# Performance work log

Measured on AMD Instinct MI355X. Metric: run time of the kernel, lower is better.

## Reference

```python
import jax, jax.numpy as jnp
import numpy as np


def setup_inputs() -> dict:
    key = jax.random.key(0)
    k1, k2, k3 = jax.random.split(key, 3)
    B, S, D = 4, 2048, 1024   # batch, seq_len, hidden
    M = 65536                 # external memory size
    x = jax.random.normal(k1, (B, S, D), dtype=jnp.float32)
    keys = jax.random.normal(k2, (M, D), dtype=jnp.float32)
    vals = jax.random.normal(k3, (M, D), dtype=jnp.float32)
    return {"x": x, "ver": 1, "keys": keys, "vals": vals}


def reference(x, ver, keys, vals):
    # linear_attention: unnormalized attention over external memory.
    #   out = (x @ keys^T) @ vals
    # Use associativity to avoid materializing the [B,S,M] score matrix:
    #   kv = keys^T @ vals  -> [D, D]
    kv = jnp.einsum("md,me->de", keys, vals)   # [D, D]
    out = jnp.einsum("bsd,de->bse", x, kv)      # [B, S, D]
    return out
```

## Files before the change

### kernel.cpp

```cpp
#include <hip/hip_runtime.h>
#include <hip/hip_bf16.h>


typedef __attribute__((ext_vector_type(8))) __bf16 bf16x8;
typedef __attribute__((ext_vector_type(4))) __bf16 bf16x4;
typedef __attribute__((ext_vector_type(4))) float  f32x4;

#define D_DIM   1024
#define M_DIM   65536
#define ROWS    8192
#define NCHUNK  16
#define MC      (M_DIM / NCHUNK)
#define BT      128
#define BK      64
#define LDK     72
#define TILE_BYTES 16384

__device__ __forceinline__ f32x4 mfma16(bf16x8 a, bf16x8 b, f32x4 c) {
    return __builtin_amdgcn_mfma_f32_16x16x32_bf16(a, b, c, 0, 0, 0);
}

__device__ __forceinline__ void gl_lds16(const void* gsrc, void* ldst) {
    __builtin_amdgcn_global_load_lds(
        (const __attribute__((address_space(1))) unsigned int*)gsrc,
        (__attribute__((address_space(3))) unsigned int*)ldst,
        16, 0, 0);
}

__global__ __launch_bounds__(256)
void convert_tile(const float* __restrict__ keys,
                  const float* __restrict__ vals,
                  __hip_bfloat16* __restrict__ KtT,
                  __hip_bfloat16* __restrict__ VtT)
{
    const float* src = blockIdx.z ? vals : keys;
    char* dstb = (char*)(blockIdx.z ? VtT : KtT);

    const int tid = threadIdx.x;
    const int s   = blockIdx.x;
    const int dq  = blockIdx.y;
    const int m0  = s * 64;
    const int d0  = dq * 256;

    const int q   = tid & 15;
    const int dcb = tid >> 4;

    const int cl   = q >> 1;
    const int half = (q & 1) << 3;

    f32x4 v[4][4];
    #pragma unroll
    for (int i = 0; i < 4; ++i) {
        const int dc = dcb + 16 * i;
        #pragma unroll
        for (int r = 0; r < 4; ++r)
            v[i][r] = *(const f32x4*)(src + (size_t)(m0 + 4 * q + r) * D_DIM + d0 + 4 * dc);
    }

    #pragma unroll
    for (int i = 0; i < 4; ++i) {
        const int dc = dcb + 16 * i;
        #pragma unroll
        for (int j = 0; j < 4; ++j) {
            bf16x4 w;
            #pragma unroll
            for (int r = 0; r < 4; ++r) w[r] = (__bf16)v[i][r][j];
            const int d  = 4 * dc + j;
            const int t  = dq * 2 + (d >> 7);
            const int dl = d & 127;
            char* tile = dstb + ((size_t)t * 1024 + s) * TILE_BYTES;
            *(bf16x4*)(tile + dl * 128 + ((cl ^ (dl & 7)) << 4) + half) = w;
        }
    }
}

__global__ __launch_bounds__(256)
void convert_rows(const float* __restrict__ src,
                  __hip_bfloat16* __restrict__ dstT)
{
    const int tid = threadIdx.x;
    const int rt  = blockIdx.x;
    const int t   = blockIdx.y;
    const int r0  = rt * 128, d0 = t * 64;
    char* tile = (char*)dstT + ((size_t)rt * 16 + t) * TILE_BYTES;
    #pragma unroll
    for (int it = 0; it < 4; ++it) {
        const int idx = tid + it * 256;
        const int r   = idx >> 3;
        const int cl  = idx & 7;
        const float* p = src + (size_t)(r0 + r) * D_DIM + d0 + cl * 8;
        f32x4 a = *(const f32x4*)p;
        f32x4 b = *(const f32x4*)(p + 4);
        bf16x8 w;
        w[0] = (__bf16)a[0]; w[1] = (__bf16)a[1]; w[2] = (__bf16)a[2]; w[3] = (__bf16)a[3];
        w[4] = (__bf16)b[0]; w[5] = (__bf16)b[1]; w[6] = (__bf16)b[2]; w[7] = (__bf16)b[3];
        *(bf16x8*)(tile + r * 128 + ((cl ^ (r & 7)) * 16)) = w;
    }
}

__global__ __launch_bounds__(512, 2)
void kv_gemm8(const __hip_bfloat16* __restrict__ VtT,
              const __hip_bfloat16* __restrict__ KtT,
              float* __restrict__ kvw)
{
    __shared__ __align__(16) char lds[2][4][TILE_BYTES];

    const int tid  = threadIdx.x;
    const int lane = tid & 63;
    const int wave = tid >> 6;
    const int we   = wave >> 2;
    const int wd   = wave & 3;

    const int bx    = blockIdx.x;
    const int xcd   = bx & 7;
    const int idx   = bx >> 3;
    const int chunk = ((idx >> 4) << 3) | xcd;
    const int t16   = idx & 15;
    const int E8    = t16 >> 2;
    const int D8    = t16 & 3;

    const size_t step0 = (size_t)chunk * 64;

    const char* Vb = (const char*)VtT;
    const char* Kb = (const char*)KtT;

    const int l15 = lane & 15;
    const int l7  = lane & 7;
    const int hi  = lane >> 4;

    f32x4 acc[8][4] = {};

    auto tileptr = [&](const char* base, int rt, int t) -> const char* {
        return base + ((size_t)rt * 1024 + step0 + (size_t)t) * TILE_BYTES;
    };
    auto stage_sub = [&](int buf, int sub, const char* tile) {
        char* dst = &lds[buf][sub][wave * 1024];
        const char* s = tile + wave * 1024 + lane * 16;
        gl_lds16(s,        dst);
        gl_lds16(s + 8192, dst + 8192);
    };

    stage_sub(0, 0, tileptr(Vb, 2 * E8,     0));
    stage_sub(0, 1, tileptr(Vb, 2 * E8 + 1, 0));
    stage_sub(0, 2, tileptr(Kb, 2 * D8,     0));
    stage_sub(0, 3, tileptr(Kb, 2 * D8 + 1, 0));
    asm volatile("s_waitcnt vmcnt(0)" ::: "memory");
    __builtin_amdgcn_s_barrier();

    bf16x8 bfr[4][2];

    #pragma unroll 2
    for (int t = 0; t < 64; ++t) {
        const int buf = t & 1;
        const char* abase = &lds[buf][we][0];
        const char* bbase = &lds[buf][2 + (wd >> 1)][0];
        const int brow0 = (wd & 1) * 64;

        #pragma unroll
        for (int p = 0; p < 4; ++p) {
            bf16x8 afr[2][2];
            #pragma unroll
            for (int j = 0; j < 2; ++j)
                #pragma unroll
                for (int ks = 0; ks < 2; ++ks) {
                    const int row = (2 * p + j) * 16 + l15;
                    afr[j][ks] = *(const bf16x8*)(abase + row * 128
                                   + (((ks << 2) + hi) ^ l7) * 16);
                }
            if (p == 0) {
                #pragma unroll
                for (int n = 0; n < 4; ++n)
                    #pragma unroll
                    for (int ks = 0; ks < 2; ++ks) {
                        const int row = brow0 + n * 16 + l15;
                        bfr[n][ks] = *(const bf16x8*)(bbase + row * 128
                                       + (((ks << 2) + hi) ^ l7) * 16);
                    }
            }
            if (p == 0 && t + 1 < 64) {
                stage_sub(buf ^ 1, 0, tileptr(Vb, 2 * E8,     t + 1));
                stage_sub(buf ^ 1, 1, tileptr(Vb, 2 * E8 + 1, t + 1));
            }
            if (p == 1 && t + 1 < 64) {
                stage_sub(buf ^ 1, 2, tileptr(Kb, 2 * D8,     t + 1));
                stage_sub(buf ^ 1, 3, tileptr(Kb, 2 * D8 + 1, t + 1));
            }
            __builtin_amdgcn_s_barrier();
            asm volatile("s_waitcnt lgkmcnt(0)" ::: "memory");
            __builtin_amdgcn_sched_barrier(0);
            __builtin_amdgcn_s_setprio(1);
            #pragma unroll
            for (int j = 0; j < 2; ++j)
                #pragma unroll
                for (int n = 0; n < 4; ++n)
                    #pragma unroll
                    for (int ks = 0; ks < 2; ++ks)
                        acc[2 * p + j][n] = mfma16(afr[j][ks], bfr[n][ks],
                                                   acc[2 * p + j][n]);
            __builtin_amdgcn_s_setprio(0);
            if (p == 3)
                asm volatile("s_waitcnt vmcnt(0)" ::: "memory");
            __builtin_amdgcn_s_barrier();
        }
    }

    const int rb = hi * 4;
    #pragma unroll
    for (int mi = 0; mi < 8; ++mi) {
        #pragma unroll
        for (int ni = 0; ni < 4; ++ni) {
            const int d = D8 * 256 + wd * 64 + ni * 16 + l15;
            #pragma unroll
            for (int r = 0; r < 4; ++r) {
                const int e = E8 * 256 + we * 128 + mi * 16 + rb + r;
                atomicAdd(kvw + (size_t)e * D_DIM + d, acc[mi][ni][r]);
            }
        }
    }
}

__global__ __launch_bounds__(512, 1)
void out_gemm8(const __hip_bfloat16* __restrict__ xbT,
               const __hip_bfloat16* __restrict__ kvbT,
               float* __restrict__ out)
{
    __shared__ __align__(16) char lds[2][3][TILE_BYTES];

    const int tid  = threadIdx.x;
    const int lane = tid & 63;
    const int wave = tid >> 6;
    const int wr   = wave >> 2;
    const int wee  = wave & 3;

    const int bx = blockIdx.x;
    const int rt = bx & 63;
    const int be = bx >> 6;

    const int l15 = lane & 15;
    const int l7  = lane & 7;
    const int hi  = lane >> 4;

    f32x4 acc[4][4] = {};

    const char* Xb = (const char*)xbT;
    const char* Kv = (const char*)kvbT;

    auto tileA = [&](int t) -> const char* {
        return Xb + ((size_t)rt * 16 + t) * TILE_BYTES;
    };
    auto tileB = [&](int j, int t) -> const char* {
        return Kv + ((size_t)(2 * be + j) * 16 + t) * TILE_BYTES;
    };
    auto stage_sub = [&](int buf, int sub, const char* tile) {
        char* dst = &lds[buf][sub][wave * 1024];
        const char* s = tile + wave * 1024 + lane * 16;
        gl_lds16(s,        dst);
        gl_lds16(s + 8192, dst + 8192);
    };

    stage_sub(0, 0, tileA(0));
    stage_sub(0, 1, tileB(0, 0));
    stage_sub(0, 2, tileB(1, 0));
    asm volatile("s_waitcnt vmcnt(0)" ::: "memory");
    __builtin_amdgcn_s_barrier();

    bf16x8 bfr[4][2];

    for (int t = 0; t < 16; ++t) {
        const int buf = t & 1;
        const char* abase = &lds[buf][0][0];
        const char* bbase = &lds[buf][1 + (wee >> 1)][0];
        const int brow0 = (wee & 1) * 64;

        #pragma unroll
        for (int p = 0; p < 4; ++p) {
            bf16x8 afr[2];
            #pragma unroll
            for (int ks = 0; ks < 2; ++ks) {
                const int row = wr * 64 + p * 16 + l15;
                afr[ks] = *(const bf16x8*)(abase + row * 128
                              + (((ks << 2) + hi) ^ l7) * 16);
            }
            if (p == 0) {
                #pragma unroll
                for (int n = 0; n < 4; ++n)
                    #pragma unroll
                    for (int ks = 0; ks < 2; ++ks) {
                        const int row = brow0 + n * 16 + l15;
                        bfr[n][ks] = *(const bf16x8*)(bbase + row * 128
                                       + (((ks << 2) + hi) ^ l7) * 16);
                    }
            }
            if (p == 0 && t + 1 < 16) stage_sub(buf ^ 1, 0, tileA(t + 1));
            if (p == 1 && t + 1 < 16) {
                stage_sub(buf ^ 1, 1, tileB(0, t + 1));
                stage_sub(buf ^ 1, 2, tileB(1, t + 1));
            }
            __builtin_amdgcn_s_barrier();
            asm volatile("s_waitcnt lgkmcnt(0)" ::: "memory");
            __builtin_amdgcn_sched_barrier(0);
            __builtin_amdgcn_s_setprio(1);
            #pragma unroll
            for (int n = 0; n < 4; ++n)
                #pragma unroll
                for (int ks = 0; ks < 2; ++ks)
                    acc[p][n] = mfma16(afr[ks], bfr[n][ks], acc[p][n]);
            __builtin_amdgcn_s_setprio(0);
            if (p == 3)
                asm volatile("s_waitcnt vmcnt(0)" ::: "memory");
            __builtin_amdgcn_s_barrier();
        }
    }

    const int r0 = rt * 128, e0 = be * 256;
    #pragma unroll
    for (int mi = 0; mi < 4; ++mi) {
        #pragma unroll
        for (int ni = 0; ni < 4; ++ni) {
            const int e = e0 + wee * 64 + ni * 16 + l15;
            #pragma unroll
            for (int r = 0; r < 4; ++r) {
                const int rr = r0 + wr * 64 + mi * 16 + hi * 4 + r;
                out[(size_t)rr * D_DIM + e] = acc[mi][ni][r];
            }
        }
    }
}

__global__ __launch_bounds__(256)
void kv_partial_kernel(const float* __restrict__ keys,
                       const float* __restrict__ vals,
                       float* __restrict__ kvw)
{
    __shared__ __bf16 Ktl[BT][LDK];
    __shared__ __bf16 Vtl[BT][LDK];

    const int tid  = threadIdx.x;
    const int lane = tid & 63;
    const int wave = tid >> 6;
    const int wr   = wave >> 1;
    const int wc   = wave & 1;

    const int tile  = blockIdx.x & 63;
    const int chunk = blockIdx.x >> 6;
    const int d0 = (tile >> 3) * BT;
    const int e0 = (tile & 7) * BT;
    const size_t mbeg = (size_t)chunk * MC;

    f32x4 acc[4][4] = {};
    const int kg  = tid & 15;
    const int d4a = tid >> 4;

    for (int ms = 0; ms < MC; ms += BK) {
        #pragma unroll
        for (int i = 0; i < 2; ++i) {
            const int dloc = (d4a + i * 16) * 4;
            const size_t mrow = mbeg + ms + (size_t)kg * 4;
            f32x4 kr[4], vr[4];
            #pragma unroll
            for (int r = 0; r < 4; ++r) {
                kr[r] = *(const f32x4*)(keys + (mrow + r) * D_DIM + d0 + dloc);
                vr[r] = *(const f32x4*)(vals + (mrow + r) * D_DIM + e0 + dloc);
            }
            #pragma unroll
            for (int j = 0; j < 4; ++j) {
                bf16x4 wk, wv;
                #pragma unroll
                for (int r = 0; r < 4; ++r) {
                    wk[r] = (__bf16)kr[r][j];
                    wv[r] = (__bf16)vr[r][j];
                }
                *(bf16x4*)&Ktl[dloc + j][kg * 4] = wk;
                *(bf16x4*)&Vtl[dloc + j][kg * 4] = wv;
            }
        }
        __syncthreads();

        #pragma unroll
        for (int ks = 0; ks < BK; ks += 32) {
            bf16x8 af[4], bf[4];
            #pragma unroll
            for (int t = 0; t < 4; ++t) {
                af[t] = *(const bf16x8*)&Ktl[wr * 64 + t * 16 + (lane & 15)][ks + (lane >> 4) * 8];
                bf[t] = *(const bf16x8*)&Vtl[wc * 64 + t * 16 + (lane & 15)][ks + (lane >> 4) * 8];
            }
            #pragma unroll
            for (int mi = 0; mi < 4; ++mi)
                #pragma unroll
                for (int ni = 0; ni < 4; ++ni)
                    acc[mi][ni] = mfma16(af[mi], bf[ni], acc[mi][ni]);
        }
        __syncthreads();
    }

    const int rbase = (lane >> 4) * 4;
    const int cidx  = lane & 15;
    #pragma unroll
    for (int mi = 0; mi < 4; ++mi) {
        #pragma unroll
        for (int ni = 0; ni < 4; ++ni) {
            const int e = e0 + wc * 64 + ni * 16 + cidx;
            #pragma unroll
            for (int reg = 0; reg < 4; ++reg) {
                const int d = d0 + wr * 64 + mi * 16 + rbase + reg;
                atomicAdd(kvw + (size_t)e * D_DIM + d, acc[mi][ni][reg]);
            }
        }
    }
}

__global__ __launch_bounds__(256)
void out_gemm_kernel(const float* __restrict__ x,
                     const float* __restrict__ kvw,
                     float* __restrict__ out)
{
    __shared__ __bf16 Xt[BT][LDK];
    __shared__ __bf16 Wt[BT][LDK];

    const int tid  = threadIdx.x;
    const int lane = tid & 63;
    const int wave = tid >> 6;
    const int wr   = wave >> 1;
    const int wc   = wave & 1;

    const int r0 = blockIdx.x * BT;
    const int e0 = blockIdx.y * BT;

    f32x4 acc[4][4] = {};

    for (int ks0 = 0; ks0 < D_DIM; ks0 += BK) {
        #pragma unroll
        for (int i = 0; i < 8; ++i) {
            const int idx = tid + i * 256;
            const int row = idx >> 4;
            const int col = (idx & 15) * 4;
            f32x4 xa = *(const f32x4*)(x   + (size_t)(r0 + row) * D_DIM + ks0 + col);
            f32x4 wa = *(const f32x4*)(kvw + (size_t)(e0 + row) * D_DIM + ks0 + col);
            bf16x4 xb, wb;
            #pragma unroll
            for (int j = 0; j < 4; ++j) {
                xb[j] = (__bf16)xa[j];
                wb[j] = (__bf16)wa[j];
            }
            *(bf16x4*)&Xt[row][col] = xb;
            *(bf16x4*)&Wt[row][col] = wb;
        }
        __syncthreads();

        #pragma unroll
        for (int ks = 0; ks < BK; ks += 32) {
            bf16x8 af[4], bf[4];
            #pragma unroll
            for (int t = 0; t < 4; ++t) {
                af[t] = *(const bf16x8*)&Xt[wr * 64 + t * 16 + (lane & 15)][ks + (lane >> 4) * 8];
                bf[t] = *(const bf16x8*)&Wt[wc * 64 + t * 16 + (lane & 15)][ks + (lane >> 4) * 8];
            }
            #pragma unroll
            for (int mi = 0; mi < 4; ++mi)
                #pragma unroll
                for (int ni = 0; ni < 4; ++ni)
                    acc[mi][ni] = mfma16(af[mi], bf[ni], acc[mi][ni]);
        }
        __syncthreads();
    }

    const int rbase = (lane >> 4) * 4;
    const int cidx  = lane & 15;
    #pragma unroll
    for (int mi = 0; mi < 4; ++mi) {
        #pragma unroll
        for (int ni = 0; ni < 4; ++ni) {
            const int e = e0 + wc * 64 + ni * 16 + cidx;
            #pragma unroll
            for (int reg = 0; reg < 4; ++reg) {
                const int r = r0 + wr * 64 + mi * 16 + rbase + reg;
                out[(size_t)r * D_DIM + e] = acc[mi][ni][reg];
            }
        }
    }
}

extern "C" void kernel_launch(void* const* d_in, const int* in_sizes, int n_in,
                              void* d_out, int out_size, void* d_ws, size_t ws_size,
                              hipStream_t stream) {
    const float* x    = (const float*)d_in[0];
    const float* keys = (const float*)d_in[2];
    const float* vals = (const float*)d_in[3];
    float* out = (float*)d_out;

    const size_t kvw_bytes = (size_t)D_DIM * D_DIM * sizeof(float);
    const size_t kt_bytes  = (size_t)D_DIM * M_DIM * sizeof(__hip_bfloat16);
    const size_t xb_bytes  = (size_t)ROWS * D_DIM * sizeof(__hip_bfloat16);
    const size_t kvb_bytes = (size_t)D_DIM * D_DIM * sizeof(__hip_bfloat16);
    const size_t need_kv   = kvw_bytes + 2 * kt_bytes;
    const size_t need_full = need_kv + xb_bytes + kvb_bytes;

    float* kvw = (float*)d_ws;
    hipMemsetAsync(kvw, 0, kvw_bytes, stream);

    if (ws_size >= need_kv) {
        __hip_bfloat16* KtT = (__hip_bfloat16*)((char*)d_ws + kvw_bytes);
        __hip_bfloat16* VtT = (__hip_bfloat16*)((char*)d_ws + kvw_bytes + kt_bytes);
        convert_tile<<<dim3(M_DIM / 64, 4, 2), dim3(256), 0, stream>>>(
            keys, vals, KtT, VtT);
        kv_gemm8<<<dim3(256), dim3(512), 0, stream>>>(VtT, KtT, kvw);

        if (ws_size >= need_full) {
            __hip_bfloat16* xbT  = (__hip_bfloat16*)((char*)d_ws + need_kv);
            __hip_bfloat16* kvbT = (__hip_bfloat16*)((char*)d_ws + need_kv + xb_bytes);
            convert_rows<<<dim3(ROWS / 128, 16), dim3(256), 0, stream>>>(x, xbT);
            convert_rows<<<dim3(D_DIM / 128, 16), dim3(256), 0, stream>>>(kvw, kvbT);
            out_gemm8<<<dim3(256), dim3(512), 0, stream>>>(xbT, kvbT, out);
        } else {
            out_gemm_kernel<<<dim3(64, 8), dim3(256), 0, stream>>>(x, kvw, out);
        }
    } else {
        kv_partial_kernel<<<dim3(64 * NCHUNK), dim3(256), 0, stream>>>(keys, vals, kvw);
        out_gemm_kernel<<<dim3(64, 8), dim3(256), 0, stream>>>(x, kvw, out);
    }
}
```

Baseline: 376.8 us.

## Fuse fp32-to-bf16 conversion of keys/vals into the kv GEMM main loop

Removes the separate convert_tile pass that wrote bf16 transposed copies of keys and vals to workspace. The new kv_gemm_fused kernel loads fp32 rows directly into registers, converts them and writes swizzled bf16 tiles into LDS inside the double-buffered GEMM loop. This avoids writing and rereading the 256MB bf16 intermediate and one launch. In exchange it drops the async global-to-LDS loads, adds register pressure and VALU conversion work per tile, and reduces occupancy to one block per CU. The workspace requirement also shrinks.

```diff
diff --git a/kernel.cpp b/kernel.cpp
--- a/kernel.cpp
+++ b/kernel.cpp
@@ -27,49 +27,142 @@
         16, 0, 0);
 }
 
-__global__ __launch_bounds__(256)
-void convert_tile(const float* __restrict__ keys,
-                  const float* __restrict__ vals,
-                  __hip_bfloat16* __restrict__ KtT,
-                  __hip_bfloat16* __restrict__ VtT)
+__global__ __launch_bounds__(512, 1)
+void kv_gemm_fused(const float* __restrict__ keys,
+                   const float* __restrict__ vals,
+                   float* __restrict__ kvw)
 {
-    const float* src = blockIdx.z ? vals : keys;
-    char* dstb = (char*)(blockIdx.z ? VtT : KtT);
-
-    const int tid = threadIdx.x;
-    const int s   = blockIdx.x;
-    const int dq  = blockIdx.y;
-    const int m0  = s * 64;
-    const int d0  = dq * 256;
-
-    const int q   = tid & 15;
-    const int dcb = tid >> 4;
-
-    const int cl   = q >> 1;
+    __shared__ __align__(16) char lds[2][4][TILE_BYTES];
+
+    const int tid  = threadIdx.x;
+    const int lane = tid & 63;
+    const int wave = tid >> 6;
+    const int we   = wave >> 2;
+    const int wd   = wave & 3;
+
+    const int bx    = blockIdx.x;
+    const int xcd   = bx & 7;
+    const int idx   = bx >> 3;
+    const int chunk = ((idx >> 4) << 3) | xcd;
+    const int t16   = idx & 15;
+    const int E8    = t16 >> 2;
+    const int D8    = t16 & 3;
+
+    const size_t mbase = (size_t)chunk * MC;
+
+    const int grp = tid >> 8;
+    const int tq  = tid & 255;
+    const int q   = tq & 15;
+    const int dcb = tq >> 4;
+    const int clq  = q >> 1;
     const int half = (q & 1) << 3;
-
+    const float* psrc = grp ? keys : vals;
+    const int c0 = (grp ? D8 : E8) * 256;
+
+    const int l15 = lane & 15;
+    const int l7  = lane & 7;
+    const int hi  = lane >> 4;
+
+    f32x4 acc[8][4] = {};
     f32x4 v[4][4];
+
+    auto stage_load = [&](int t) {
+        #pragma unroll
+        for (int i = 0; i < 4; ++i) {
+            const int cq = dcb + 16 * i;
+            #pragma unroll
+            for (int r = 0; r < 4; ++r)
+                v[i][r] = *(const f32x4*)(psrc
+                    + (mbase + (size_t)t * BK + 4 * q + r) * D_DIM + c0 + 4 * cq);
+        }
+    };
+    auto stage_write = [&](int buf) {
+        #pragma unroll
+        for (int i = 0; i < 4; ++i) {
+            const int cq = dcb + 16 * i;
+            #pragma unroll
+            for (int j = 0; j < 4; ++j) {
+                bf16x4 w;
+                #pragma unroll
+                for (int r = 0; r < 4; ++r) w[r] = (__bf16)v[i][r][j];
+                const int row = 4 * cq + j;
+                const int sub = 2 * grp + (row >> 7);
+                const int dl  = row & 127;
+                *(bf16x4*)(&lds[buf][sub][0] + dl * 128
+                           + ((clq ^ (dl & 7)) << 4) + half) = w;
+            }
+        }
+    };
+
+    stage_load(0);
+    asm volatile("s_waitcnt vmcnt(0)" ::: "memory");
+    stage_write(0);
+    asm volatile("s_waitcnt lgkmcnt(0)" ::: "memory");
+    __builtin_amdgcn_s_barrier();
+
+    bf16x8 bfr[4][2];
+
+    for (int t = 0; t < 64; ++t) {
+        const int buf = t & 1;
+        const char* abase = &lds[buf][we][0];
+        const char* bbase = &lds[buf][2 + (wd >> 1)][0];
+        const int brow0 = (wd & 1) * 64;
+
+        #pragma unroll
+        for (int p = 0; p < 4; ++p) {
+            bf16x8 afr[2][2];
+            #pragma unroll
+            for (int j = 0; j < 2; ++j)
+                #pragma unroll
+                for (int ks = 0; ks < 2; ++ks) {
+                    const int row = (2 * p + j) * 16 + l15;
+                    afr[j][ks] = *(const bf16x8*)(abase + row * 128
+                                   + (((ks << 2) + hi) ^ l7) * 16);
+                }
+            if (p == 0) {
+                #pragma unroll
+                for (int n = 0; n < 4; ++n)
+                    #pragma unroll
+                    for (int ks = 0; ks < 2; ++ks) {
+                        const int row = brow0 + n * 16 + l15;
+                        bfr[n][ks] = *(const bf16x8*)(bbase + row * 128
+                                       + (((ks << 2) + hi) ^ l7) * 16);
+                    }
+                if (t + 1 < 64) stage_load(t + 1);
+            }
+            __builtin_amdgcn_s_barrier();
+            asm volatile("s_waitcnt lgkmcnt(0)" ::: "memory");
+            __builtin_amdgcn_sched_barrier(0);
+            __builtin_amdgcn_s_setprio(1);
+            #pragma unroll
+            for (int j = 0; j < 2; ++j)
+                #pragma unroll
+                for (int n = 0; n < 4; ++n)
+                    #pragma unroll
+                    for (int ks = 0; ks < 2; ++ks)
+                        acc[2 * p + j][n] = mfma16(afr[j][ks], bfr[n][ks],
+                                                   acc[2 * p + j][n]);
+            __builtin_amdgcn_s_setprio(0);
+            if (p == 3 && t + 1 < 64) {
+                asm volatile("s_waitcnt vmcnt(0)" ::: "memory");
+                stage_write(buf ^ 1);
+                asm volatile("s_waitcnt lgkmcnt(0)" ::: "memory");
+            }
+            __builtin_amdgcn_s_barrier();
+        }
+    }
+
+    const int rb = hi * 4;
     #pragma unroll
-    for (int i = 0; i < 4; ++i) {
-        const int dc = dcb + 16 * i;
-        #pragma unroll
-        for (int r = 0; r < 4; ++r)
-            v[i][r] = *(const f32x4*)(src + (size_t)(m0 + 4 * q + r) * D_DIM + d0 + 4 * dc);
-    }
-
-    #pragma unroll
-    for (int i = 0; i < 4; ++i) {
-        const int dc = dcb + 16 * i;
-        #pragma unroll
-        for (int j = 0; j < 4; ++j) {
-            bf16x4 w;
-            #pragma unroll
-            for (int r = 0; r < 4; ++r) w[r] = (__bf16)v[i][r][j];
-            const int d  = 4 * dc + j;
-            const int t  = dq * 2 + (d >> 7);
-            const int dl = d & 127;
-            char* tile = dstb + ((size_t)t * 1024 + s) * TILE_BYTES;
-            *(bf16x4*)(tile + dl * 128 + ((cl ^ (dl & 7)) << 4) + half) = w;
+    for (int mi = 0; mi < 8; ++mi) {
+        #pragma unroll
+        for (int ni = 0; ni < 4; ++ni) {
+            const int d = D8 * 256 + wd * 64 + ni * 16 + l15;
+            #pragma unroll
+            for (int r = 0; r < 4; ++r) {
+                const int e = E8 * 256 + we * 128 + mi * 16 + rb + r;
+                atomicAdd(kvw + (size_t)e * D_DIM + d, acc[mi][ni][r]);
+            }
         }
     }
 }
@@ -98,127 +191,6 @@
     }
 }
 
-__global__ __launch_bounds__(512, 2)
-void kv_gemm8(const __hip_bfloat16* __restrict__ VtT,
-              const __hip_bfloat16* __restrict__ KtT,
-              float* __restrict__ kvw)
-{
-    __shared__ __align__(16) char lds[2][4][TILE_BYTES];
-
-    const int tid  = threadIdx.x;
-    const int lane = tid & 63;
-    const int wave = tid >> 6;
-    const int we   = wave >> 2;
-    const int wd   = wave & 3;
-
-    const int bx    = blockIdx.x;
-    const int xcd   = bx & 7;
-    const int idx   = bx >> 3;
-    const int chunk = ((idx >> 4) << 3) | xcd;
-    const int t16   = idx & 15;
-    const int E8    = t16 >> 2;
-    const int D8    = t16 & 3;
-
-    const size_t step0 = (size_t)chunk * 64;
-
-    const char* Vb = (const char*)VtT;
-    const char* Kb = (const char*)KtT;
-
-    const int l15 = lane & 15;
-    const int l7  = lane & 7;
-    const int hi  = lane >> 4;
-
-    f32x4 acc[8][4] = {};
-
-    auto tileptr = [&](const char* base, int rt, int t) -> const char* {
-        return base + ((size_t)rt * 1024 + step0 + (size_t)t) * TILE_BYTES;
-    };
-    auto stage_sub = [&](int buf, int sub, const char* tile) {
-        char* dst = &lds[buf][sub][wave * 1024];
-        const char* s = tile + wave * 1024 + lane * 16;
-        gl_lds16(s,        dst);
-        gl_lds16(s + 8192, dst + 8192);
-    };
-
-    stage_sub(0, 0, tileptr(Vb, 2 * E8,     0));
-    stage_sub(0, 1, tileptr(Vb, 2 * E8 + 1, 0));
-    stage_sub(0, 2, tileptr(Kb, 2 * D8,     0));
-    stage_sub(0, 3, tileptr(Kb, 2 * D8 + 1, 0));
-    asm volatile("s_waitcnt vmcnt(0)" ::: "memory");
-    __builtin_amdgcn_s_barrier();
-
-    bf16x8 bfr[4][2];
-
-    #pragma unroll 2
-    for (int t = 0; t < 64; ++t) {
-        const int buf = t & 1;
-        const char* abase = &lds[buf][we][0];
-        const char* bbase = &lds[buf][2 + (wd >> 1)][0];
-        const int brow0 = (wd & 1) * 64;
-
-        #pragma unroll
-        for (int p = 0; p < 4; ++p) {
-            bf16x8 afr[2][2];
-            #pragma unroll
-            for (int j = 0; j < 2; ++j)
-                #pragma unroll
-                for (int ks = 0; ks < 2; ++ks) {
-                    const int row = (2 * p + j) * 16 + l15;
-                    afr[j][ks] = *(const bf16x8*)(abase + row * 128
-                                   + (((ks << 2) + hi) ^ l7) * 16);
-                }
-            if (p == 0) {
-                #pragma unroll
-                for (int n = 0; n < 4; ++n)
-                    #pragma unroll
-                    for (int ks = 0; ks < 2; ++ks) {
-                        const int row = brow0 + n * 16 + l15;
-                        bfr[n][ks] = *(const bf16x8*)(bbase + row * 128
-                                       + (((ks << 2) + hi) ^ l7) * 16);
-                    }
-            }
-            if (p == 0 && t + 1 < 64) {
-                stage_sub(buf ^ 1, 0, tileptr(Vb, 2 * E8,     t + 1));
-                stage_sub(buf ^ 1, 1, tileptr(Vb, 2 * E8 + 1, t + 1));
-            }
-            if (p == 1 && t + 1 < 64) {
-                stage_sub(buf ^ 1, 2, tileptr(Kb, 2 * D8,     t + 1));
-                stage_sub(buf ^ 1, 3, tileptr(Kb, 2 * D8 + 1, t + 1));
-            }
-            __builtin_amdgcn_s_barrier();
-            asm volatile("s_waitcnt lgkmcnt(0)" ::: "memory");
-            __builtin_amdgcn_sched_barrier(0);
-            __builtin_amdgcn_s_setprio(1);
-            #pragma unroll
-            for (int j = 0; j < 2; ++j)
-                #pragma unroll
-                for (int n = 0; n < 4; ++n)
-                    #pragma unroll
-                    for (int ks = 0; ks < 2; ++ks)
-                        acc[2 * p + j][n] = mfma16(afr[j][ks], bfr[n][ks],
-                                                   acc[2 * p + j][n]);
-            __builtin_amdgcn_s_setprio(0);
-            if (p == 3)
-                asm volatile("s_waitcnt vmcnt(0)" ::: "memory");
-            __builtin_amdgcn_s_barrier();
-        }
-    }
-
-    const int rb = hi * 4;
-    #pragma unroll
-    for (int mi = 0; mi < 8; ++mi) {
-        #pragma unroll
-        for (int ni = 0; ni < 4; ++ni) {
-            const int d = D8 * 256 + wd * 64 + ni * 16 + l15;
-            #pragma unroll
-            for (int r = 0; r < 4; ++r) {
-                const int e = E8 * 256 + we * 128 + mi * 16 + rb + r;
-                atomicAdd(kvw + (size_t)e * D_DIM + d, acc[mi][ni][r]);
-            }
-        }
-    }
-}
-
 __global__ __launch_bounds__(512, 1)
 void out_gemm8(const __hip_bfloat16* __restrict__ xbT,
                const __hip_bfloat16* __restrict__ kvbT,
@@ -489,31 +461,20 @@
     float* out = (float*)d_out;
 
     const size_t kvw_bytes = (size_t)D_DIM * D_DIM * sizeof(float);
-    const size_t kt_bytes  = (size_t)D_DIM * M_DIM * sizeof(__hip_bfloat16);
     const size_t xb_bytes  = (size_t)ROWS * D_DIM * sizeof(__hip_bfloat16);
     const size_t kvb_bytes = (size_t)D_DIM * D_DIM * sizeof(__hip_bfloat16);
-    const size_t need_kv   = kvw_bytes + 2 * kt_bytes;
-    const size_t need_full = need_kv + xb_bytes + kvb_bytes;
+    const size_t need_fused = kvw_bytes + xb_bytes + kvb_bytes;
 
     float* kvw = (float*)d_ws;
     hipMemsetAsync(kvw, 0, kvw_bytes, stream);
 
-    if (ws_size >= need_kv) {
-        __hip_bfloat16* KtT = (__hip_bfloat16*)((char*)d_ws + kvw_bytes);
-        __hip_bfloat16* VtT = (__hip_bfloat16*)((char*)d_ws + kvw_bytes + kt_bytes);
-        convert_tile<<<dim3(M_DIM / 64, 4, 2), dim3(256), 0, stream>>>(
-            keys, vals, KtT, VtT);
-        kv_gemm8<<<dim3(256), dim3(512), 0, stream>>>(VtT, KtT, kvw);
-
-        if (ws_size >= need_full) {
-            __hip_bfloat16* xbT  = (__hip_bfloat16*)((char*)d_ws + need_kv);
-            __hip_bfloat16* kvbT = (__hip_bfloat16*)((char*)d_ws + need_kv + xb_bytes);
-            convert_rows<<<dim3(ROWS / 128, 16), dim3(256), 0, stream>>>(x, xbT);
-            convert_rows<<<dim3(D_DIM / 128, 16), dim3(256), 0, stream>>>(kvw, kvbT);
-            out_gemm8<<<dim3(256), dim3(512), 0, stream>>>(xbT, kvbT, out);
-        } else {
-            out_gemm_kernel<<<dim3(64, 8), dim3(256), 0, stream>>>(x, kvw, out);
-        }
+    if (ws_size >= need_fused) {
+        __hip_bfloat16* xbT  = (__hip_bfloat16*)((char*)d_ws + kvw_bytes);
+        __hip_bfloat16* kvbT = (__hip_bfloat16*)((char*)d_ws + kvw_bytes + xb_bytes);
+        kv_gemm_fused<<<dim3(256), dim3(512), 0, stream>>>(keys, vals, kvw);
+        convert_rows<<<dim3(ROWS / 128, 16), dim3(256), 0, stream>>>(x, xbT);
+        convert_rows<<<dim3(D_DIM / 128, 16), dim3(256), 0, stream>>>(kvw, kvbT);
+        out_gemm8<<<dim3(256), dim3(512), 0, stream>>>(xbT, kvbT, out);
     } else {
         kv_partial_kernel<<<dim3(64 * NCHUNK), dim3(256), 0, stream>>>(keys, vals, kvw);
         out_gemm_kernel<<<dim3(64, 8), dim3(256), 0, stream>>>(x, kvw, out);
```

After: 650.0 us. 1.72x slower.
